# Kernel optimization log

Hardware: AMD Instinct MI355X
Metric: run time of the kernel (lower is better)

Reference implementation:

```python
import jax, jax.numpy as jnp
import numpy as np

B, S, D, V = 4, 1024, 512, 8192
SCALES = [1, 2, 4, 8, 16]   # nn.Parameter init; used via int(scale.item()) -> static
WIN = 8                     # min(8, S//2) in compute_semantic_coherence
EPS = 1e-5


def layer_norm(x, g, b):
    m = x.mean(-1, keepdims=True)
    v = ((x - m) ** 2).mean(-1, keepdims=True)
    return (x - m) / jnp.sqrt(v + EPS) * g + b


def setup_inputs() -> dict:
    key = jax.random.key(0)
    ks = jax.random.split(key, 24)
    n = lambda k, shape, s=0.02: (jax.random.normal(k, shape, jnp.float32) * s)
    return {
        "embeddings": jax.random.normal(ks[0], (B, S, D), jnp.float32),
        "token_ids": jax.random.randint(ks[1], (B, S), 0, V),
        "context_mask": jnp.ones((B, S), jnp.float32),
        "token_similarity": n(ks[2], (V, V)),
        "W_scale": n(ks[3], (len(SCALES), D), 0.05), "b_scale": jnp.zeros((D,), jnp.float32),
        "W_sem": n(ks[4], (1, D), 0.05), "b_sem": jnp.zeros((D,), jnp.float32),
        "W_ctx": n(ks[5], (D, D), 0.02), "b_ctx": jnp.zeros((D,), jnp.float32),
        "W_fuse": n(ks[6], (4 * D, D), 0.02), "b_fuse": jnp.zeros((D,), jnp.float32),
        "ln1_g": jnp.ones((D,), jnp.float32), "ln1_b": jnp.zeros((D,), jnp.float32),
        "ln2_g": jnp.ones((D,), jnp.float32), "ln2_b": jnp.zeros((D,), jnp.float32),
        "ln3_g": jnp.ones((D,), jnp.float32), "ln3_b": jnp.zeros((D,), jnp.float32),
        "W_e0": n(ks[7], (D, D), 0.02), "b_e0": jnp.zeros((D,), jnp.float32),
        "W_e1": n(ks[8], (D, D), 0.02), "b_e1": jnp.zeros((D,), jnp.float32),
        "W_e2": n(ks[9], (D, D), 0.02), "b_e2": jnp.zeros((D,), jnp.float32),
    }


def _forward(embeddings, token_ids, context_mask, token_similarity,
             W_scale, b_scale, W_sem, b_sem, W_ctx, b_ctx, W_fuse, b_fuse,
             ln1_g, ln1_b, ln2_g, ln2_b, ln3_g, ln3_b,
             W_e0, b_e0, W_e1, b_e1, W_e2, b_e2):
    phases = jnp.tanh(embeddings)  # [B,S,D]

    # --- multi-scale coherence via cumulative sums + cos angle-difference identity ---
    # mean_t cos(p_t - m) = cos(m)*mean(cos p) + sin(m)*mean(sin p) over each window
    z = jnp.zeros((B, 1, D), phases.dtype)
    cum_p = jnp.concatenate([z, jnp.cumsum(phases, 1)], 1)            # [B,S+1,D]
    cum_c = jnp.concatenate([z, jnp.cumsum(jnp.cos(phases), 1)], 1)
    cum_s = jnp.concatenate([z, jnp.cumsum(jnp.sin(phases), 1)], 1)
    cols = []
    for s in SCALES:
        wm = (cum_p[:, s:] - cum_p[:, :-s]) / s   # window mean  [B,S-s+1,D]
        ac = (cum_c[:, s:] - cum_c[:, :-s]) / s   # window mean cos
        asn = (cum_s[:, s:] - cum_s[:, :-s]) / s  # window mean sin
        coh = jnp.mean(jnp.cos(wm) * ac + jnp.sin(wm) * asn, -1)      # [B,S-s+1]
        cols.append(jnp.pad(coh, ((0, 0), (0, s - 1))))               # torch leaves tail zeros
    msc = jnp.stack(cols, -1)                                         # [B,S,num_scales]
    scale_coh = msc @ W_scale + b_scale                               # [B,S,D]

    # --- semantic coherence (windowed, sim-weighted; torch takes mean over WHOLE tensor incl. batch) ---
    te = token_similarity[token_ids]                                  # [B,S,V]
    ten = te / jnp.maximum(jnp.linalg.norm(te, axis=-1, keepdims=True), 1e-12)
    tsim = jnp.einsum('biv,bjv->bij', ten, ten)                       # [B,S,S]
    off = jnp.arange(-WIN, WIN + 1)
    pos = jnp.arange(S)[:, None] + off[None, :]                       # [S,17]
    valid = (pos >= 0) & (pos < S)
    posc = jnp.clip(pos, 0, S - 1)
    pwin = phases[:, posc]                                            # [B,S,17,D]
    swin = jnp.take_along_axis(tsim, jnp.broadcast_to(posc[None], (B, S, 2 * WIN + 1)), axis=2)
    coh = jnp.cos((phases[:, :, None, :] - pwin) * swin[..., None]) * valid[None, :, :, None].astype(phases.dtype)
    counts = valid.sum(1).astype(phases.dtype)                        # [S]
    sem = coh.sum((0, 2, 3)) / (B * counts * D)                       # [S] (same scalar for all batches)
    sem = jnp.broadcast_to(sem[None, :], (B, S))[..., None]           # [B,S,1]
    sem_coh = sem @ W_sem + b_sem                                     # [B,S,D]

    # --- context coherence (context_mask path) ---
    cmean = jnp.mean(embeddings * context_mask[..., None], 1, keepdims=True)
    ctx_coh = jnp.cos(embeddings - cmean) @ W_ctx + b_ctx

    # --- local coherence ---
    lc = jnp.cos(embeddings[:, 1:] - embeddings[:, :-1])
    lc = jnp.concatenate([lc, jnp.zeros((B, 1, D), embeddings.dtype)], 1)

    allc = jnp.concatenate([scale_coh, sem_coh, ctx_coh, lc], -1)     # [B,S,4D]
    x = layer_norm(allc @ W_fuse + b_fuse, ln1_g, ln1_b)
    x = jax.nn.gelu(x, approximate=False)                             # dropout = identity (eval)
    for W, bb in ((W_e0, b_e0), (W_e1, b_e1), (W_e2, b_e2)):
        r = x
        h = layer_norm(x, ln2_g, ln2_b) @ W + bb
        x = r + jax.nn.gelu(h, approximate=False) * 0.1
    return layer_norm(x, ln3_g, ln3_b)


def reference(embeddings, token_ids, context_mask, token_similarity,
              W_scale, b_scale, W_sem, b_sem, W_ctx, b_ctx, W_fuse, b_fuse,
              ln1_g, ln1_b, ln2_g, ln2_b, ln3_g, ln3_b,
              W_e0, b_e0, W_e1, b_e1, W_e2, b_e2):
    return _forward(embeddings, token_ids, context_mask, token_similarity,
                    W_scale, b_scale, W_sem, b_sem, W_ctx, b_ctx, W_fuse, b_fuse,
                    ln1_g, ln1_b, ln2_g, ln2_b, ln3_g, ln3_b,
                    W_e0, b_e0, W_e1, b_e1, W_e2, b_e2)
```

## Files before the change

### kernel.cpp

```cpp
#include <hip/hip_runtime.h>


#define DEV __device__ __forceinline__
typedef unsigned short u16;
typedef __bf16 bf16x8 __attribute__((ext_vector_type(8)));
typedef float f32x4 __attribute__((ext_vector_type(4)));

static constexpr int S = 1024;
static constexpr int D = 512;
static constexpr int KCAT = 1088;

DEV u16 f2bf(float f) {
  unsigned u = __float_as_uint(f);
  return (u16)((u + 0x7fffu + ((u >> 16) & 1u)) >> 16);
}
DEV float bf2f(u16 v) { return __uint_as_float((unsigned)v << 16); }
DEV float gelu(float x) { return 0.5f * x * (1.f + erff(x * 0.70710678118654752f)); }
DEV float wredx(float v) {
#pragma unroll
  for (int m = 32; m; m >>= 1) v += __shfl_xor(v, m, 64);
  return v;
}
DEV float qred(float v) {
  v += __shfl_xor(v, 1, 64);
  v += __shfl_xor(v, 2, 64);
  return v;
}

__global__ __launch_bounds__(256) void k_front(
    const float* __restrict__ emb, const float* __restrict__ mask,
    float* __restrict__ ph, float* __restrict__ cmacc,
    const float* __restrict__ sim, const int* __restrict__ tok,
    float* __restrict__ dots_raw, float* __restrict__ normsq,
    const float* __restrict__ W0, const float* __restrict__ W1,
    const float* __restrict__ W2, const float* __restrict__ Wf,
    const float* __restrict__ wctx, const float* __restrict__ Wsc,
    const float* __restrict__ Wsm, const float* __restrict__ bsc,
    const float* __restrict__ bsm, const float* __restrict__ bcx,
    u16* __restrict__ T0, u16* __restrict__ T1, u16* __restrict__ T2,
    u16* __restrict__ wcatT, float* __restrict__ ctx_acc,
    float* __restrict__ sm_acc) {
  __shared__ __align__(16) float smem[9360];
  __shared__ int stok[72];
  int blk = blockIdx.x, tid = threadIdx.x;

  if (blk < 1024) {
    int bx = blk >> 4, cyb = blk & 15;
    int b = bx >> 4, g0 = (bx & 15) * 64, gidx = b * S + g0;
    if (tid < 72) {
      int pp = g0 + tid;
      stok[tid] = (pp < S) ? tok[b * S + pp] : -1;
    }
    __syncthreads();
    const float4* sim4 = (const float4*)sim;
    f32x4* sT4 = (f32x4*)smem;
    int wave = tid >> 6, lane = tid & 63;
    int p = lane & 31, h = lane >> 5;
    int qb = wave * 8 + h * 4;
    const f32x4* bj[10];
#pragma unroll
    for (int j = 0; j < 10; ++j)
      bj[j] = sT4 + (p + (j >> 1)) * 65 + 2 * qb + (j & 1);
    f32x4 ac0[9] = {}, ac1[9] = {};
    for (int cc = 0; cc < 4; ++cc) {
      int cy = cyb * 4 + cc;
#pragma unroll
      for (int it = 0; it < 9; ++it) {
        int u = it * 256 + tid, r = u >> 5, q = u & 31;
        int tk = stok[r];
        float4 v = make_float4(0.f, 0.f, 0.f, 0.f);
        if (tk >= 0) v = sim4[(size_t)tk * 2048 + cy * 32 + q];
        f32x4 vv = {v.x, v.y, v.z, v.w};
        sT4[(r >> 1) * 65 + 2 * q + (r & 1)] = vv;
      }
      __syncthreads();
#pragma unroll
      for (int c4 = 0; c4 < 4; ++c4) {
        f32x4 v0 = bj[0][2 * c4], v1 = bj[1][2 * c4], v2 = bj[2][2 * c4],
              v3 = bj[3][2 * c4], v4 = bj[4][2 * c4], v5 = bj[5][2 * c4],
              v6 = bj[6][2 * c4], v7 = bj[7][2 * c4], v8 = bj[8][2 * c4],
              v9 = bj[9][2 * c4];
        ac0[8] += v0 * v0;  ac1[8] += v1 * v1;
        ac0[0] += v0 * v1;  ac1[0] += v1 * v2;
        ac0[1] += v0 * v2;  ac1[1] += v1 * v3;
        ac0[2] += v0 * v3;  ac1[2] += v1 * v4;
        ac0[3] += v0 * v4;  ac1[3] += v1 * v5;
        ac0[4] += v0 * v5;  ac1[4] += v1 * v6;
        ac0[5] += v0 * v6;  ac1[5] += v1 * v7;
        ac0[6] += v0 * v7;  ac1[6] += v1 * v8;
        ac0[7] += v0 * v8;  ac1[7] += v1 * v9;
      }
      __syncthreads();
    }
    float* red = smem;
#pragma unroll
    for (int s = 0; s < 9; ++s) {
      f32x4 a = ac0[s], c = ac1[s];
      red[(wave * 9 + s) * 128 + h * 64 + 2 * p]     = a[0] + a[1] + a[2] + a[3];
      red[(wave * 9 + s) * 128 + h * 64 + 2 * p + 1] = c[0] + c[1] + c[2] + c[3];
    }
    __syncthreads();
    for (int u = tid; u < 576; u += 256) {
      int s = u >> 6, a = u & 63;
      float v = 0.f;
#pragma unroll
      for (int wh = 0; wh < 8; ++wh)
        v += red[((wh >> 1) * 9 + s) * 128 + (wh & 1) * 64 + a];
      if (s < 8) atomicAdd(&dots_raw[(size_t)(gidx + a) * 8 + s], v);
      else       atomicAdd(&normsq[gidx + a], v);
    }
    return;
  }

  if (blk < 2080) {
    int blk2 = blk - 1024;
    if (blk2 < 1024) {
      int idx = blk2 * 256 + tid;
#pragma unroll
      for (int r = 0; r < 2; ++r, idx += 262144) {
        float4 v = ((const float4*)emb)[idx];
        float4 o;
        o.x = tanhf(v.x); o.y = tanhf(v.y); o.z = tanhf(v.z); o.w = tanhf(v.w);
        ((float4*)ph)[idx] = o;
      }
    } else {
      int r = blk2 - 1024, b = r >> 3, chunk = r & 7;
      float a0 = 0.f, a1 = 0.f;
      for (int s = chunk * 128; s < chunk * 128 + 128; ++s) {
        float m = mask[b * S + s];
        const float* row = emb + (size_t)(b * S + s) * D;
        a0 += row[tid] * m; a1 += row[tid + 256] * m;
      }
      atomicAdd(cmacc + b * D + tid, a0);
      atomicAdd(cmacc + b * D + tid + 256, a1);
    }
    return;
  }

  int blk2 = blk - 2080;
  if (blk2 < 256) {
    int z = blk2 >> 6, rem = blk2 & 63;
    const float* src = z == 0 ? W0 : z == 1 ? W1 : z == 2 ? W2 : Wf + (size_t)1536 * 512;
    int r0 = (rem >> 3) * 64, c0 = (rem & 7) * 64;
    int tr = tid >> 6, tc = tid & 63;
#pragma unroll 4
    for (int i = 0; i < 16; ++i)
      smem[(tr + i * 4) * 65 + tc] = src[(size_t)(r0 + tr + i * 4) * 512 + c0 + tc];
    __syncthreads();
#pragma unroll 4
    for (int i = 0; i < 16; ++i) {
      int n = c0 + tr + i * 4, k = r0 + tc;
      u16 v = f2bf(smem[tc * 65 + tr + i * 4]);
      if (z == 3) wcatT[(size_t)n * KCAT + 512 + k] = v;
      else (z == 0 ? T0 : z == 1 ? T1 : T2)[(size_t)n * 512 + k] = v;
    }
  } else if (blk2 < 512) {
    int rem = blk2 - 256;
    int n = (rem & 1) * 256 + tid;
    int kbase = ((rem & 63) >> 1) * 16;
    int j0 = (rem >> 6) * 128;
    float acc[16] = {};
    for (int j = j0; j < j0 + 128; ++j) {
      float wf3 = Wf[(size_t)(1024 + j) * 512 + n];
#pragma unroll
      for (int kk = 0; kk < 16; ++kk) acc[kk] += wctx[(size_t)(kbase + kk) * 512 + j] * wf3;
    }
#pragma unroll
    for (int kk = 0; kk < 16; ++kk)
      atomicAdd(&ctx_acc[(size_t)(kbase + kk) * 512 + n], acc[kk]);
  } else {
    int rem = blk2 - 512;
    int n = (rem & 1) * 256 + tid;
    int j0 = (rem >> 1) * 16;
    float a0 = 0.f, a1 = 0.f, a2 = 0.f, a3 = 0.f, a4 = 0.f, au = 0.f, ac = 0.f;
    for (int j = j0; j < j0 + 16; ++j) {
      float wf1 = Wf[(size_t)j * 512 + n];
      float wf2 = Wf[(size_t)(512 + j) * 512 + n];
      float wf3 = Wf[(size_t)(1024 + j) * 512 + n];
      a0 += Wsc[j] * wf1; a1 += Wsc[512 + j] * wf1; a2 += Wsc[1024 + j] * wf1;
      a3 += Wsc[1536 + j] * wf1; a4 += Wsc[2048 + j] * wf1;
      au += Wsm[j] * wf2;
      ac += bsc[j] * wf1 + bsm[j] * wf2 + bcx[j] * wf3;
    }
    atomicAdd(&sm_acc[0 * 512 + n], a0);
    atomicAdd(&sm_acc[1 * 512 + n], a1);
    atomicAdd(&sm_acc[2 * 512 + n], a2);
    atomicAdd(&sm_acc[3 * 512 + n], a3);
    atomicAdd(&sm_acc[4 * 512 + n], a4);
    atomicAdd(&sm_acc[5 * 512 + n], au);
    atomicAdd(&sm_acc[6 * 512 + n], ac);
  }
}

static constexpr int CP2 = 68;
__global__ __launch_bounds__(256) void k_mid(const float* __restrict__ ph,
    const float* __restrict__ dots_raw, const float* __restrict__ normsq,
    float* __restrict__ msc_raw, float* __restrict__ semacc,
    const float* __restrict__ ctx_acc, const float* __restrict__ sm_acc,
    const float* __restrict__ bfu, u16* __restrict__ wcatT) {
  __shared__ __align__(16) float smem[7072];
  int blk = blockIdx.x, tid = threadIdx.x;

  if (blk < 512) {
    float* sP = smem;
    float* sw2 = smem + 88 * CP2;
    int bx = blk >> 3, dy = blk & 7;
    int b = bx >> 4, g0 = (bx & 15) * 64;
    const float4* ph4 = (const float4*)ph;
#pragma unroll
    for (int it = 0; it < 6; ++it) {
      int u = it * 256 + tid;
      if (u < 1408) {
        int r = u >> 4, q = u & 15;
        int gr = g0 - 8 + r;
        gr = gr < 0 ? 0 : (gr > S - 1 ? S - 1 : gr);
        float4 v = ph4[(size_t)(b * S + gr) * 128 + dy * 16 + q];
        *(float4*)&sP[r * CP2 + 4 * q] = v;
      }
    }
    for (int u = tid; u < 1088; u += 256) {
      int a = u / 17, oi = u - a * 17;
      int i = g0 + a, o = oi - 8, j = i + o;
      int idx = b * S + i;
      float v = 0.f;
      if (j >= 0 && j < S) {
        if (o == 0) v = 1.f;
        else {
          float dr = (o > 0) ? dots_raw[(size_t)idx * 8 + o - 1]
                             : dots_raw[(size_t)(idx + o) * 8 + (-o - 1)];
          float ni = fmaxf(sqrtf(normsq[idx]), 1e-12f);
          float nj = fmaxf(sqrtf(normsq[idx + o]), 1e-12f);
          v = dr / (ni * nj);
        }
      }
      sw2[u] = v;
    }
    __syncthreads();
    int ar = tid >> 2, dq = tid & 3;
    int i = g0 + ar, idx = b * S + i;
    int jmax = S - 1 - i; if (jmax > 15) jmax = 15;
    float swr[17];
#pragma unroll
    for (int oi = 0; oi < 17; ++oi) swr[oi] = sw2[ar * 17 + oi];
    float a0 = 0.f, a1 = 0.f, a2 = 0.f, a3 = 0.f, a4 = 0.f, asem = 0.f;
#pragma unroll 2
    for (int dd = 0; dd < 16; ++dd) {
      int d = dq + 4 * dd;
      const float* pb = &sP[(ar + 8) * CP2 + d];
      float sp = 0.f, sc = 0.f, ss = 0.f;
#pragma unroll
      for (int j = 0; j < 16; ++j) {
        float x = (j <= jmax) ? pb[j * CP2] : 0.f;
        sp += x; sc += __cosf(x); ss += __sinf(x);
        if (j == 0) a0 += __cosf(sp) * sc + __sinf(sp) * ss;
        else if (j == 1)  { float wm = sp * 0.5f;    a1 += __cosf(wm) * (sc * 0.5f)    + __sinf(wm) * (ss * 0.5f); }
        else if (j == 3)  { float wm = sp * 0.25f;   a2 += __cosf(wm) * (sc * 0.25f)   + __sinf(wm) * (ss * 0.25f); }
        else if (j == 7)  { float wm = sp * 0.125f;  a3 += __cosf(wm) * (sc * 0.125f)  + __sinf(wm) * (ss * 0.125f); }
        else if (j == 15) { float wm = sp * 0.0625f; a4 += __cosf(wm) * (sc * 0.0625f) + __sinf(wm) * (ss * 0.0625f); }
      }
      float p0 = pb[0];
      const float* qb = &sP[ar * CP2 + d];
#pragma unroll
      for (int oi = 0; oi < 17; ++oi) {
        int j = i + oi - 8;
        bool valid = (j >= 0) && (j < S);
        float pj = qb[oi * CP2];
        asem += valid ? __cosf((p0 - pj) * swr[oi]) : 0.f;
      }
    }
    a0 = qred(a0); a1 = qred(a1); a2 = qred(a2); a3 = qred(a3); a4 = qred(a4);
    asem = qred(asem);
    if (dq == 0) {
      float* mr = msc_raw + (size_t)idx * 5;
      atomicAdd(mr + 0, a0); atomicAdd(mr + 1, a1); atomicAdd(mr + 2, a2);
      atomicAdd(mr + 3, a3); atomicAdd(mr + 4, a4);
      atomicAdd(semacc + i, asem);
    }
    return;
  }

  int blk2 = blk - 512;
  if (blk2 < 64) {
    int r0 = (blk2 >> 3) * 64, c0 = (blk2 & 7) * 64;
    int tr = tid >> 6, tc = tid & 63;
#pragma unroll 4
    for (int i = 0; i < 16; ++i)
      smem[(tr + i * 4) * 65 + tc] = ctx_acc[(size_t)(r0 + tr + i * 4) * 512 + c0 + tc];
    __syncthreads();
#pragma unroll 4
    for (int i = 0; i < 16; ++i)
      wcatT[(size_t)(c0 + tr + i * 4) * KCAT + r0 + tc] = f2bf(smem[tc * 65 + tr + i * 4]);
  } else {
    int n = (blk2 - 64) * 256 + tid;
    u16* row = wcatT + (size_t)n * KCAT;
#pragma unroll
    for (int s = 0; s < 6; ++s) row[1024 + s] = f2bf(sm_acc[s * 512 + n]);
    row[1030] = f2bf(sm_acc[6 * 512 + n] + bfu[n]);
    for (int k = 1031; k < KCAT; ++k) row[k] = 0;
  }
}

__global__ __launch_bounds__(256) void k_xcat(const float* __restrict__ emb,
    const float* __restrict__ cmacc, const float* __restrict__ msc_raw,
    const float* __restrict__ semacc, u16* __restrict__ xcat) {
  int idx = blockIdx.x, b = idx >> 10, i = idx & 1023, tid = threadIdx.x;
  const float* erow = emb + (size_t)idx * D;
  u16* orow = xcat + (size_t)idx * KCAT;
  for (int c = tid; c < KCAT; c += 256) {
    float v;
    if (c < 512) {
      v = __cosf(erow[c] - cmacc[b * D + c] * (1.f / 1024.f));
    } else if (c < 1024) {
      int d = c - 512;
      v = (i < S - 1) ? __cosf(erow[D + d] - erow[d]) : 0.f;
    } else if (c < 1029) {
      int s = c - 1024, req = (1 << s) - 1;
      v = (S - 1 - i >= req) ? msc_raw[(size_t)idx * 5 + s] * (1.f / 512.f) : 0.f;
    } else if (c == 1029) {
      int cnt = ((i < 8) ? i : 8) + ((S - 1 - i < 8) ? (S - 1 - i) : 8) + 1;
      v = semacc[i] / (4.f * (float)cnt * 512.f);
    } else if (c == 1030) {
      v = 1.f;
    } else v = 0.f;
    orow[c] = f2bf(v);
  }
}

__global__ __launch_bounds__(256) void k_gemm(const u16* __restrict__ A,
    const u16* __restrict__ BT, float* __restrict__ Cf, u16* __restrict__ Cb,
    const float* __restrict__ bias, int K, int obf) {
  __shared__ __align__(16) u16 sA[64 * 72];
  __shared__ __align__(16) u16 sB[64 * 72];
  int tid = threadIdx.x, wave = tid >> 6, lane = tid & 63;
  int m0 = blockIdx.x * 64, n0 = blockIdx.y * 64;
  int lr = tid >> 2, lc = (tid & 3) * 8;
  int q8 = (lane >> 4) * 8, l15 = lane & 15;
  const u16* Ap = A + (size_t)(m0 + lr) * K + lc;
  const u16* Bp = BT + (size_t)(n0 + lr) * K + lc;
  uint4 ra0 = *(const uint4*)(Ap);
  uint4 ra1 = *(const uint4*)(Ap + 32);
  uint4 rb0 = *(const uint4*)(Bp);
  uint4 rb1 = *(const uint4*)(Bp + 32);
  f32x4 acc[4] = {};
  for (int k0 = 0; k0 < K; k0 += 64) {
    *(uint4*)&sA[lr * 72 + lc]      = ra0;
    *(uint4*)&sA[lr * 72 + lc + 32] = ra1;
    *(uint4*)&sB[lr * 72 + lc]      = rb0;
    *(uint4*)&sB[lr * 72 + lc + 32] = rb1;
    __syncthreads();
    if (k0 + 64 < K) {
      ra0 = *(const uint4*)(Ap + k0 + 64);
      ra1 = *(const uint4*)(Ap + k0 + 96);
      rb0 = *(const uint4*)(Bp + k0 + 64);
      rb1 = *(const uint4*)(Bp + k0 + 96);
    }
    int row = wave * 16 + l15;
    bf16x8 af0 = *(const bf16x8*)&sA[row * 72 + q8];
    bf16x8 af1 = *(const bf16x8*)&sA[row * 72 + 32 + q8];
#pragma unroll
    for (int f = 0; f < 4; ++f) {
      bf16x8 b0 = *(const bf16x8*)&sB[(f * 16 + l15) * 72 + q8];
      bf16x8 b1 = *(const bf16x8*)&sB[(f * 16 + l15) * 72 + 32 + q8];
      acc[f] = __builtin_amdgcn_mfma_f32_16x16x32_bf16(af0, b0, acc[f], 0, 0, 0);
      acc[f] = __builtin_amdgcn_mfma_f32_16x16x32_bf16(af1, b1, acc[f], 0, 0, 0);
    }
    __syncthreads();
  }
  int r0 = m0 + wave * 16 + (lane >> 4) * 4;
#pragma unroll
  for (int f = 0; f < 4; ++f) {
    int col = n0 + f * 16 + l15;
    float bv = bias ? bias[col] : 0.f;
#pragma unroll
    for (int r = 0; r < 4; ++r) {
      float cv = acc[f][r] + bv;
      if (obf) Cb[(size_t)(r0 + r) * 512 + col] = f2bf(cv);
      else     Cf[(size_t)(r0 + r) * 512 + col] = cv;
    }
  }
}

__global__ __launch_bounds__(256) void k_post_y1(const float* __restrict__ y,
    float* __restrict__ x, u16* __restrict__ t,
    const float* __restrict__ g1, const float* __restrict__ b1,
    const float* __restrict__ g2, const float* __restrict__ b2) {
  int tid = threadIdx.x, w = tid >> 6, lane = tid & 63;
  int row = blockIdx.x * 4 + w;
  size_t base = (size_t)row * 512 + lane * 8;
  int gb = lane * 8;
  float4 va = *(const float4*)(y + base);
  float4 vb = *(const float4*)(y + base + 4);
  float v[8] = {va.x, va.y, va.z, va.w, vb.x, vb.y, vb.z, vb.w};
  float s = 0.f, ss = 0.f;
#pragma unroll
  for (int k = 0; k < 8; ++k) { s += v[k]; ss += v[k] * v[k]; }
  s = wredx(s); ss = wredx(ss);
  float m = s * (1.f / 512.f);
  float inv = rsqrtf(ss * (1.f / 512.f) - m * m + 1e-5f);
  float4 gA = *(const float4*)(g1 + gb), gB = *(const float4*)(g1 + gb + 4);
  float4 bA = *(const float4*)(b1 + gb), bB = *(const float4*)(b1 + gb + 4);
  float gv[8] = {gA.x, gA.y, gA.z, gA.w, gB.x, gB.y, gB.z, gB.w};
  float bv[8] = {bA.x, bA.y, bA.z, bA.w, bB.x, bB.y, bB.z, bB.w};
  float xv[8];
  float s2 = 0.f, ss2 = 0.f;
#pragma unroll
  for (int k = 0; k < 8; ++k) {
    xv[k] = gelu((v[k] - m) * inv * gv[k] + bv[k]);
    s2 += xv[k]; ss2 += xv[k] * xv[k];
  }
  *(float4*)(x + base)     = make_float4(xv[0], xv[1], xv[2], xv[3]);
  *(float4*)(x + base + 4) = make_float4(xv[4], xv[5], xv[6], xv[7]);
  s2 = wredx(s2); ss2 = wredx(ss2);
  m = s2 * (1.f / 512.f);
  inv = rsqrtf(ss2 * (1.f / 512.f) - m * m + 1e-5f);
  float4 g2A = *(const float4*)(g2 + gb), g2B = *(const float4*)(g2 + gb + 4);
  float4 b2A = *(const float4*)(b2 + gb), b2B = *(const float4*)(b2 + gb + 4);
  float g2v[8] = {g2A.x, g2A.y, g2A.z, g2A.w, g2B.x, g2B.y, g2B.z, g2B.w};
  float b2v[8] = {b2A.x, b2A.y, b2A.z, b2A.w, b2B.x, b2B.y, b2B.z, b2B.w};
  union { u16 us[8]; uint4 u4; } pk;
#pragma unroll
  for (int k = 0; k < 8; ++k) pk.us[k] = f2bf((xv[k] - m) * inv * g2v[k] + b2v[k]);
  *(uint4*)(t + base) = pk.u4;
}

__global__ __launch_bounds__(256) void k_post_res(const u16* __restrict__ hb,
    float* __restrict__ x, u16* __restrict__ t, float* __restrict__ out,
    const float* __restrict__ g, const float* __restrict__ bb, int final_) {
  int tid = threadIdx.x, w = tid >> 6, lane = tid & 63;
  int row = blockIdx.x * 4 + w;
  size_t base = (size_t)row * 512 + lane * 8;
  int gb = lane * 8;
  union { u16 us[8]; uint4 u4; } hk;
  hk.u4 = *(const uint4*)(hb + base);
  float4 xa = *(const float4*)(x + base);
  float4 xb = *(const float4*)(x + base + 4);
  float xv[8] = {xa.x, xa.y, xa.z, xa.w, xb.x, xb.y, xb.z, xb.w};
  float s = 0.f, ss = 0.f;
#pragma unroll
  for (int k = 0; k < 8; ++k) {
    xv[k] += 0.1f * gelu(bf2f(hk.us[k]));
    s += xv[k]; ss += xv[k] * xv[k];
  }
  s = wredx(s); ss = wredx(ss);
  float m = s * (1.f / 512.f);
  float inv = rsqrtf(ss * (1.f / 512.f) - m * m + 1e-5f);
  float4 gA = *(const float4*)(g + gb), gB = *(const float4*)(g + gb + 4);
  float4 bA = *(const float4*)(bb + gb), bB = *(const float4*)(bb + gb + 4);
  float gv[8] = {gA.x, gA.y, gA.z, gA.w, gB.x, gB.y, gB.z, gB.w};
  float bv[8] = {bA.x, bA.y, bA.z, bA.w, bB.x, bB.y, bB.z, bB.w};
  float nv[8];
#pragma unroll
  for (int k = 0; k < 8; ++k) nv[k] = (xv[k] - m) * inv * gv[k] + bv[k];
  if (final_) {
    *(float4*)(out + base)     = make_float4(nv[0], nv[1], nv[2], nv[3]);
    *(float4*)(out + base + 4) = make_float4(nv[4], nv[5], nv[6], nv[7]);
  } else {
    *(float4*)(x + base)     = make_float4(xv[0], xv[1], xv[2], xv[3]);
    *(float4*)(x + base + 4) = make_float4(xv[4], xv[5], xv[6], xv[7]);
    union { u16 us[8]; uint4 u4; } pk;
#pragma unroll
    for (int k = 0; k < 8; ++k) pk.us[k] = f2bf(nv[k]);
    *(uint4*)(t + base) = pk.u4;
  }
}

extern "C" void kernel_launch(void* const* d_in, const int* in_sizes, int n_in,
                              void* d_out, int out_size, void* d_ws, size_t ws_size,
                              hipStream_t stream) {
  const float* emb     = (const float*)d_in[0];
  const int*   tok     = (const int*)d_in[1];
  const float* mask    = (const float*)d_in[2];
  const float* sim     = (const float*)d_in[3];
  const float* W_scale = (const float*)d_in[4];
  const float* b_scale = (const float*)d_in[5];
  const float* W_sem   = (const float*)d_in[6];
  const float* b_sem   = (const float*)d_in[7];
  const float* W_ctx   = (const float*)d_in[8];
  const float* b_ctx   = (const float*)d_in[9];
  const float* W_fuse  = (const float*)d_in[10];
  const float* b_fuse  = (const float*)d_in[11];
  const float* ln1_g = (const float*)d_in[12], *ln1_b = (const float*)d_in[13];
  const float* ln2_g = (const float*)d_in[14], *ln2_b = (const float*)d_in[15];
  const float* ln3_g = (const float*)d_in[16], *ln3_b = (const float*)d_in[17];
  const float* W_e0 = (const float*)d_in[18], *b_e0 = (const float*)d_in[19];
  const float* W_e1 = (const float*)d_in[20], *b_e1 = (const float*)d_in[21];
  const float* W_e2 = (const float*)d_in[22], *b_e2 = (const float*)d_in[23];
  float* out = (float*)d_out;

  char* w = (char*)d_ws; size_t off = 0;
  auto alloc = [&](size_t bytes) { void* p = w + off; off += (bytes + 255) & ~(size_t)255; return p; };
  float* phases = (float*)alloc((size_t)4096 * 512 * 4);
  float* hbuf   = (float*)alloc((size_t)4096 * 512 * 4);
  float* xbuf   = (float*)alloc((size_t)4096 * 512 * 4);
  u16*   tbuf   = (u16*)  alloc((size_t)4096 * 512 * 2);
  u16*   hb16   = (u16*)  alloc((size_t)4096 * 512 * 2);
  u16*   xcat   = (u16*)  alloc((size_t)4096 * KCAT * 2);
  u16*   wcatT  = (u16*)  alloc((size_t)512 * KCAT * 2);
  u16*   We0T   = (u16*)  alloc((size_t)512 * 512 * 2);
  u16*   We1T   = (u16*)  alloc((size_t)512 * 512 * 2);
  u16*   We2T   = (u16*)  alloc((size_t)512 * 512 * 2);
  float* semacc   = (float*)alloc((size_t)1024 * 4);
  float* cmacc    = (float*)alloc((size_t)4 * 512 * 4);
  float* dots_raw = (float*)alloc((size_t)4096 * 8 * 4);
  float* normsq   = (float*)alloc((size_t)4096 * 4);
  float* msc_raw  = (float*)alloc((size_t)4096 * 5 * 4);
  float* ctx_acc  = (float*)alloc((size_t)512 * 512 * 4);
  float* sm_acc   = (float*)alloc((size_t)7 * 512 * 4);
  (void)ws_size; (void)in_sizes; (void)n_in; (void)out_size;

  size_t zbytes = (size_t)(1024 + 4 * 512 + 4096 * 8 + 4096 + 4096 * 5 + 512 * 512 + 7 * 512) * 4;
  hipMemsetAsync(semacc, 0, zbytes, stream);

  k_front<<<2656, 256, 0, stream>>>(emb, mask, phases, cmacc,
                                    sim, tok, dots_raw, normsq,
                                    W_e0, W_e1, W_e2, W_fuse, W_ctx,
                                    W_scale, W_sem, b_scale, b_sem, b_ctx,
                                    We0T, We1T, We2T, wcatT, ctx_acc, sm_acc);
  k_mid<<<578, 256, 0, stream>>>(phases, dots_raw, normsq, msc_raw, semacc,
                                 ctx_acc, sm_acc, b_fuse, wcatT);

  k_xcat<<<4096, 256, 0, stream>>>(emb, cmacc, msc_raw, semacc, xcat);
  k_gemm<<<dim3(64, 8), 256, 0, stream>>>(xcat, wcatT, hbuf, nullptr, nullptr, KCAT, 0);
  k_post_y1<<<1024, 256, 0, stream>>>(hbuf, xbuf, tbuf, ln1_g, ln1_b, ln2_g, ln2_b);

  k_gemm<<<dim3(64, 8), 256, 0, stream>>>(tbuf, We0T, nullptr, hb16, b_e0, 512, 1);
  k_post_res<<<1024, 256, 0, stream>>>(hb16, xbuf, tbuf, nullptr, ln2_g, ln2_b, 0);
  k_gemm<<<dim3(64, 8), 256, 0, stream>>>(tbuf, We1T, nullptr, hb16, b_e1, 512, 1);
  k_post_res<<<1024, 256, 0, stream>>>(hb16, xbuf, tbuf, nullptr, ln2_g, ln2_b, 0);
  k_gemm<<<dim3(64, 8), 256, 0, stream>>>(tbuf, We2T, nullptr, hb16, b_e2, 512, 1);
  k_post_res<<<1024, 256, 0, stream>>>(hb16, xbuf, nullptr, out, ln3_g, ln3_b, 1);
}
```

Measured before the change: 553.6 us.

## Fuse encoder-layer GEMM with bias, GELU residual and LayerNorm epilogue

Replaces each encoder layer's separate GEMM and post-processing kernel with one kernel where a block computes 16 full output rows. Bias, GELU, residual update and LayerNorm happen in the GEMM epilogue, with a cross-wave reduction through shared memory. This removes the bf16 intermediate buffer round-trip and three kernel launches. In exchange, each block rereads the full weight matrix from global/L2 with smaller row tiles, so the GEMM has less reuse.

```diff
diff --git a/kernel.cpp b/kernel.cpp
--- a/kernel.cpp
+++ b/kernel.cpp
@@ -27,6 +27,7 @@
   return v;
 }
 
+static constexpr int CP = 132;
 __global__ __launch_bounds__(256) void k_front(
     const float* __restrict__ emb, const float* __restrict__ mask,
     float* __restrict__ ph, float* __restrict__ cmacc,
@@ -327,8 +328,7 @@
 }
 
 __global__ __launch_bounds__(256) void k_gemm(const u16* __restrict__ A,
-    const u16* __restrict__ BT, float* __restrict__ Cf, u16* __restrict__ Cb,
-    const float* __restrict__ bias, int K, int obf) {
+    const u16* __restrict__ BT, float* __restrict__ C, int K) {
   __shared__ __align__(16) u16 sA[64 * 72];
   __shared__ __align__(16) u16 sB[64 * 72];
   int tid = threadIdx.x, wave = tid >> 6, lane = tid & 63;
@@ -370,12 +370,107 @@
 #pragma unroll
   for (int f = 0; f < 4; ++f) {
     int col = n0 + f * 16 + l15;
-    float bv = bias ? bias[col] : 0.f;
+#pragma unroll
+    for (int r = 0; r < 4; ++r)
+      C[(size_t)(r0 + r) * 512 + col] = acc[f][r];
+  }
+}
+
+__global__ __launch_bounds__(512) void k_elayer(const u16* __restrict__ A,
+    const u16* __restrict__ BT, const float* __restrict__ bias,
+    float* __restrict__ x, u16* __restrict__ t, float* __restrict__ out,
+    const float* __restrict__ g, const float* __restrict__ bb, int final_) {
+  __shared__ __align__(16) u16 sA[16 * 520];
+  __shared__ float sred[2][16][8];
+  int tid = threadIdx.x, w = tid >> 6, lane = tid & 63;
+  int l15 = lane & 15, q = lane >> 4, q8 = q * 8;
+  int m0 = blockIdx.x * 16;
+#pragma unroll
+  for (int it = 0; it < 2; ++it) {
+    int u = it * 512 + tid, row = u >> 6, c8 = (u & 63) * 8;
+    *(uint4*)&sA[row * 520 + c8] = *(const uint4*)(A + (size_t)(m0 + row) * 512 + c8);
+  }
+  __syncthreads();
+  const u16* Bb = BT + (size_t)(w * 64 + l15) * 512 + q8;
+  uint4 p0[4], p1[4];
+#pragma unroll
+  for (int f = 0; f < 4; ++f) {
+    p0[f] = *(const uint4*)(Bb + f * 8192);
+    p1[f] = *(const uint4*)(Bb + f * 8192 + 32);
+  }
+  f32x4 acc[4] = {};
+  for (int k0 = 0; k0 < 512; k0 += 64) {
+    uint4 c0[4], c1[4];
+#pragma unroll
+    for (int f = 0; f < 4; ++f) { c0[f] = p0[f]; c1[f] = p1[f]; }
+    if (k0 + 64 < 512) {
+#pragma unroll
+      for (int f = 0; f < 4; ++f) {
+        p0[f] = *(const uint4*)(Bb + f * 8192 + k0 + 64);
+        p1[f] = *(const uint4*)(Bb + f * 8192 + k0 + 96);
+      }
+    }
+    bf16x8 af0 = *(const bf16x8*)&sA[l15 * 520 + k0 + q8];
+    bf16x8 af1 = *(const bf16x8*)&sA[l15 * 520 + k0 + 32 + q8];
+#pragma unroll
+    for (int f = 0; f < 4; ++f) {
+      acc[f] = __builtin_amdgcn_mfma_f32_16x16x32_bf16(af0, *(bf16x8*)&c0[f], acc[f], 0, 0, 0);
+      acc[f] = __builtin_amdgcn_mfma_f32_16x16x32_bf16(af1, *(bf16x8*)&c1[f], acc[f], 0, 0, 0);
+    }
+  }
+  float xv[4][4], s[4] = {}, ss[4] = {};
+#pragma unroll
+  for (int f = 0; f < 4; ++f) {
+    int col = w * 64 + f * 16 + l15;
+    float bv = bias[col];
 #pragma unroll
     for (int r = 0; r < 4; ++r) {
-      float cv = acc[f][r] + bv;
-      if (obf) Cb[(size_t)(r0 + r) * 512 + col] = f2bf(cv);
-      else     Cf[(size_t)(r0 + r) * 512 + col] = cv;
+      int row = q * 4 + r;
+      float xn = x[(size_t)(m0 + row) * 512 + col] + 0.1f * gelu(acc[f][r] + bv);
+      xv[f][r] = xn; s[r] += xn; ss[r] += xn * xn;
+    }
+  }
+#pragma unroll
+  for (int r = 0; r < 4; ++r) {
+#pragma unroll
+    for (int m = 1; m <= 8; m <<= 1) {
+      s[r]  += __shfl_xor(s[r],  m, 64);
+      ss[r] += __shfl_xor(ss[r], m, 64);
+    }
+  }
+  if (l15 == 0) {
+#pragma unroll
+    for (int r = 0; r < 4; ++r) {
+      sred[0][q * 4 + r][w] = s[r];
+      sred[1][q * 4 + r][w] = ss[r];
+    }
+  }
+  __syncthreads();
+  float mr[4], ir[4];
+#pragma unroll
+  for (int r = 0; r < 4; ++r) {
+    int row = q * 4 + r;
+    float st = 0.f, sst = 0.f;
+#pragma unroll
+    for (int ww = 0; ww < 8; ++ww) { st += sred[0][row][ww]; sst += sred[1][row][ww]; }
+    float m = st * (1.f / 512.f);
+    mr[r] = m;
+    ir[r] = rsqrtf(sst * (1.f / 512.f) - m * m + 1e-5f);
+  }
+#pragma unroll
+  for (int f = 0; f < 4; ++f) {
+    int col = w * 64 + f * 16 + l15;
+    float gv = g[col], bbv = bb[col];
+#pragma unroll
+    for (int r = 0; r < 4; ++r) {
+      int row = q * 4 + r;
+      float nv = (xv[f][r] - mr[r]) * ir[r] * gv + bbv;
+      if (final_) {
+        out[(size_t)(m0 + row) * 512 + col] = nv;
+      } else {
+        x[(size_t)(m0 + row) * 512 + col] = xv[f][r];
+        t[(size_t)(m0 + row) * 512 + col] = f2bf(nv);
+      }
     }
   }
 }
@@ -421,47 +516,6 @@
 #pragma unroll
   for (int k = 0; k < 8; ++k) pk.us[k] = f2bf((xv[k] - m) * inv * g2v[k] + b2v[k]);
   *(uint4*)(t + base) = pk.u4;
-}
-
-__global__ __launch_bounds__(256) void k_post_res(const u16* __restrict__ hb,
-    float* __restrict__ x, u16* __restrict__ t, float* __restrict__ out,
-    const float* __restrict__ g, const float* __restrict__ bb, int final_) {
-  int tid = threadIdx.x, w = tid >> 6, lane = tid & 63;
-  int row = blockIdx.x * 4 + w;
-  size_t base = (size_t)row * 512 + lane * 8;
-  int gb = lane * 8;
-  union { u16 us[8]; uint4 u4; } hk;
-  hk.u4 = *(const uint4*)(hb + base);
-  float4 xa = *(const float4*)(x + base);
-  float4 xb = *(const float4*)(x + base + 4);
-  float xv[8] = {xa.x, xa.y, xa.z, xa.w, xb.x, xb.y, xb.z, xb.w};
-  float s = 0.f, ss = 0.f;
-#pragma unroll
-  for (int k = 0; k < 8; ++k) {
-    xv[k] += 0.1f * gelu(bf2f(hk.us[k]));
-    s += xv[k]; ss += xv[k] * xv[k];
-  }
-  s = wredx(s); ss = wredx(ss);
-  float m = s * (1.f / 512.f);
-  float inv = rsqrtf(ss * (1.f / 512.f) - m * m + 1e-5f);
-  float4 gA = *(const float4*)(g + gb), gB = *(const float4*)(g + gb + 4);
-  float4 bA = *(const float4*)(bb + gb), bB = *(const float4*)(bb + gb + 4);
-  float gv[8] = {gA.x, gA.y, gA.z, gA.w, gB.x, gB.y, gB.z, gB.w};
-  float bv[8] = {bA.x, bA.y, bA.z, bA.w, bB.x, bB.y, bB.z, bB.w};
-  float nv[8];
-#pragma unroll
-  for (int k = 0; k < 8; ++k) nv[k] = (xv[k] - m) * inv * gv[k] + bv[k];
-  if (final_) {
-    *(float4*)(out + base)     = make_float4(nv[0], nv[1], nv[2], nv[3]);
-    *(float4*)(out + base + 4) = make_float4(nv[4], nv[5], nv[6], nv[7]);
-  } else {
-    *(float4*)(x + base)     = make_float4(xv[0], xv[1], xv[2], xv[3]);
-    *(float4*)(x + base + 4) = make_float4(xv[4], xv[5], xv[6], xv[7]);
-    union { u16 us[8]; uint4 u4; } pk;
-#pragma unroll
-    for (int k = 0; k < 8; ++k) pk.us[k] = f2bf(nv[k]);
-    *(uint4*)(t + base) = pk.u4;
-  }
 }
 
 extern "C" void kernel_launch(void* const* d_in, const int* in_sizes, int n_in,
@@ -493,7 +547,6 @@
   float* hbuf   = (float*)alloc((size_t)4096 * 512 * 4);
   float* xbuf   = (float*)alloc((size_t)4096 * 512 * 4);
   u16*   tbuf   = (u16*)  alloc((size_t)4096 * 512 * 2);
-  u16*   hb16   = (u16*)  alloc((size_t)4096 * 512 * 2);
   u16*   xcat   = (u16*)  alloc((size_t)4096 * KCAT * 2);
   u16*   wcatT  = (u16*)  alloc((size_t)512 * KCAT * 2);
   u16*   We0T   = (u16*)  alloc((size_t)512 * 512 * 2);
@@ -520,13 +573,13 @@
                                  ctx_acc, sm_acc, b_fuse, wcatT);
 
   k_xcat<<<4096, 256, 0, stream>>>(emb, cmacc, msc_raw, semacc, xcat);
-  k_gemm<<<dim3(64, 8), 256, 0, stream>>>(xcat, wcatT, hbuf, nullptr, nullptr, KCAT, 0);
+  k_gemm<<<dim3(64, 8), 256, 0, stream>>>(xcat, wcatT, hbuf, KCAT);
   k_post_y1<<<1024, 256, 0, stream>>>(hbuf, xbuf, tbuf, ln1_g, ln1_b, ln2_g, ln2_b);
 
-  k_gemm<<<dim3(64, 8), 256, 0, stream>>>(tbuf, We0T, nullptr, hb16, b_e0, 512, 1);
-  k_post_res<<<1024, 256, 0, stream>>>(hb16, xbuf, tbuf, nullptr, ln2_g, ln2_b, 0);
-  k_gemm<<<dim3(64, 8), 256, 0, stream>>>(tbuf, We1T, nullptr, hb16, b_e1, 512, 1);
-  k_post_res<<<1024, 256, 0, stream>>>(hb16, xbuf, tbuf, nullptr, ln2_g, ln2_b, 0);
-  k_gemm<<<dim3(64, 8), 256, 0, stream>>>(tbuf, We2T, nullptr, hb16, b_e2, 512, 1);
-  k_post_res<<<1024, 256, 0, stream>>>(hb16, xbuf, nullptr, out, ln3_g, ln3_b, 1);
-}
+  k_elayer<<<256, 512, 0, stream>>>(tbuf, We0T, b_e0, xbuf, tbuf, nullptr,
+                                    ln2_g, ln2_b, 0);
+  k_elayer<<<256, 512, 0, stream>>>(tbuf, We1T, b_e1, xbuf, tbuf, nullptr,
+                                    ln2_g, ln2_b, 0);
+  k_elayer<<<256, 512, 0, stream>>>(tbuf, We2T, b_e2, xbuf, nullptr, out,
+                                    ln3_g, ln3_b, 1);
+}
```

Result: slower. 574.1 us (+3.7%).
